# Optimization experiments

Measured on AMD Instinct MI355X. Metric: run time of the kernel, lower is better.

## Reference

```python
import jax, jax.numpy as jnp
import numpy as np

D_MODEL = 1024
N_HEADS = 16
D_HEAD = D_MODEL // N_HEADS
B, T = 4, 2048


def setup_inputs() -> dict:
    key = jax.random.key(0)
    ks = jax.random.split(key, 7)
    s = 0.02
    q = jax.random.normal(ks[0], (B, T, D_MODEL), dtype=jnp.float32)
    k = jax.random.normal(ks[1], (B, T, D_MODEL), dtype=jnp.float32)
    v = jax.random.normal(ks[2], (B, T, D_MODEL), dtype=jnp.float32)
    # causal mask, True = masked (strict upper triangle)
    mask = jnp.triu(jnp.ones((T, T), dtype=bool), k=1)[None, None, :, :]
    Wq = jax.random.normal(ks[3], (D_MODEL, D_MODEL), dtype=jnp.float32) * s
    Wk = jax.random.normal(ks[4], (D_MODEL, D_MODEL), dtype=jnp.float32) * s
    Wv = jax.random.normal(ks[5], (D_MODEL, D_MODEL), dtype=jnp.float32) * s
    Wo = jax.random.normal(ks[6], (D_MODEL, D_MODEL), dtype=jnp.float32) * s
    return {"q": q, "k": k, "v": v, "mask": mask,
            "Wq": Wq, "Wk": Wk, "Wv": Wv, "Wo": Wo}


def reference(q, k, v, mask, Wq, Wk, Wv, Wo):
    H, Dh = N_HEADS, D_HEAD
    scale = Dh ** -0.5

    def split(t):  # [B,T,D] -> [B,H,T,Dh]
        Bt, Tt, _ = t.shape
        return t.reshape(Bt, Tt, H, Dh).transpose(0, 2, 1, 3)

    # torch Linear (no bias): y = x @ W.T
    Q = split(q @ Wq.T)
    K = split(k @ Wk.T)
    V = split(v @ Wv.T)

    scores = jnp.einsum('bhqd,bhkd->bhqk', Q, K) * scale
    scores = jnp.where(mask, -jnp.inf, scores)
    attn = jax.nn.softmax(scores, axis=-1)
    attn = jnp.nan_to_num(attn)  # fully-masked rows -> 0
    out = jnp.einsum('bhqk,bhkd->bhqd', attn, V)
    out = out.transpose(0, 2, 1, 3).reshape(q.shape[0], q.shape[1], H * Dh)
    return out @ Wo.T
```

## Files before the change

### kernel.cpp

```cpp
#include <hip/hip_runtime.h>
#include <stdint.h>

#define D_MODEL 1024
#define N_HEADS 16
#define D_HEAD 64
#define BATCH 4
#define SEQ 2048
#define MTOT (BATCH * SEQ)

typedef unsigned short u16;
typedef __attribute__((ext_vector_type(8))) short bf16x8;
typedef __attribute__((ext_vector_type(4))) float f32x4;

#define MFMA(a, b, c) __builtin_amdgcn_mfma_f32_16x16x32_bf16((a), (b), (c), 0, 0, 0)

static __device__ __forceinline__ u16 f2bf(float f) {
  unsigned u = __builtin_bit_cast(unsigned, f);
  u += 0x7fffu + ((u >> 16) & 1u);
  return (u16)(u >> 16);
}

static __device__ __forceinline__ void gload_lds16(const void* g, void* l) {
  __builtin_amdgcn_global_load_lds(
      (const __attribute__((address_space(1))) void*)g,
      (__attribute__((address_space(3))) void*)l, 16, 0, 0);
}

__global__ __launch_bounds__(256) void cvt3(const float* __restrict__ a,
                                            const float* __restrict__ b,
                                            const float* __restrict__ c,
                                            u16* __restrict__ oa, u16* __restrict__ ob,
                                            u16* __restrict__ oc) {
  const int z = blockIdx.y;
  const float* in = (z == 0) ? a : (z == 1) ? b : c;
  u16* out = (z == 0) ? oa : (z == 1) ? ob : oc;
  int i = blockIdx.x * 256 + threadIdx.x;
  float4 v = ((const float4*)in)[i];
  ushort4 o;
  o.x = f2bf(v.x); o.y = f2bf(v.y); o.z = f2bf(v.z); o.w = f2bf(v.w);
  ((ushort4*)out)[i] = o;
}

__global__ __launch_bounds__(256) void cvt4(const float* __restrict__ a,
                                            const float* __restrict__ b,
                                            const float* __restrict__ c,
                                            const float* __restrict__ d,
                                            u16* __restrict__ oa, u16* __restrict__ ob,
                                            u16* __restrict__ oc, u16* __restrict__ od) {
  const int z = blockIdx.y;
  const float* in = (z == 0) ? a : (z == 1) ? b : (z == 2) ? c : d;
  u16* out = (z == 0) ? oa : (z == 1) ? ob : (z == 2) ? oc : od;
  int i = blockIdx.x * 256 + threadIdx.x;
  float4 v = ((const float4*)in)[i];
  ushort4 o;
  o.x = f2bf(v.x); o.y = f2bf(v.y); o.z = f2bf(v.z); o.w = f2bf(v.w);
  ((ushort4*)out)[i] = o;
}

__global__ __launch_bounds__(256) void gemm_qkv(const u16* __restrict__ xq,
                                                const u16* __restrict__ xk,
                                                const u16* __restrict__ xv,
                                                const u16* __restrict__ Wqb,
                                                const u16* __restrict__ Wkb,
                                                const u16* __restrict__ Wvb,
                                                u16* __restrict__ Qb, u16* __restrict__ Kb,
                                                u16* __restrict__ Vtg, int zbase) {
  __shared__ u16 As[128 * 64];
  __shared__ u16 Bs[128 * 64];
  const int z = blockIdx.z + zbase;
  const u16* A = (z == 0) ? xq : (z == 1) ? xk : xv;
  const u16* B = (z == 0) ? Wqb : (z == 1) ? Wkb : Wvb;

  const int t = threadIdx.x;
  const int lane = t & 63, wave = t >> 6;
  const int wm = wave & 1, wn = wave >> 1;
  const int lrow = lane & 15, quad = lane >> 4;
  const int m0 = blockIdx.x * 128, n0 = blockIdx.y * 128;
  const int srow = t >> 3, scol = (t & 7) * 8;

  f32x4 acc[4][4];
#pragma unroll
  for (int i = 0; i < 4; i++)
#pragma unroll
    for (int j = 0; j < 4; j++) acc[i][j] = (f32x4){0.f, 0.f, 0.f, 0.f};

  for (int k0 = 0; k0 < 1024; k0 += 64) {
#pragma unroll
    for (int r = 0; r < 4; ++r) {
      int rr = r * 32 + srow;
      gload_lds16(A + (size_t)(m0 + rr) * 1024 + k0 + scol, As + rr * 64 + scol);
      gload_lds16(B + (size_t)(n0 + rr) * 1024 + k0 + scol, Bs + rr * 64 + scol);
    }
    __syncthreads();
#pragma unroll
    for (int ks = 0; ks < 2; ++ks) {
      const int kk = ks * 32 + quad * 8;
      bf16x8 a[4], b[4];
#pragma unroll
      for (int i = 0; i < 4; i++)
        a[i] = *(const bf16x8*)(As + (wm * 64 + i * 16 + lrow) * 64 + kk);
#pragma unroll
      for (int j = 0; j < 4; j++)
        b[j] = *(const bf16x8*)(Bs + (wn * 64 + j * 16 + lrow) * 64 + kk);
#pragma unroll
      for (int i = 0; i < 4; i++)
#pragma unroll
        for (int j = 0; j < 4; j++) acc[i][j] = MFMA(a[i], b[j], acc[i][j]);
    }
    __syncthreads();
  }
  if (z == 2) {
    const int b = m0 >> 11;
    const int t0 = (m0 & 2047);
#pragma unroll
    for (int i = 0; i < 4; i++) {
      const int trow = t0 + wm * 64 + i * 16 + quad * 4;
#pragma unroll
      for (int j = 0; j < 4; j++) {
        const int n = n0 + wn * 64 + j * 16 + lrow;
        ushort4 pk;
        pk.x = f2bf(acc[i][j][0]); pk.y = f2bf(acc[i][j][1]);
        pk.z = f2bf(acc[i][j][2]); pk.w = f2bf(acc[i][j][3]);
        *(ushort4*)(Vtg + (size_t)b * D_MODEL * SEQ + (size_t)n * SEQ + trow) = pk;
      }
    }
  } else {
    u16* C = z ? Kb : Qb;
#pragma unroll
    for (int i = 0; i < 4; i++) {
      const int mr = m0 + wm * 64 + i * 16 + quad * 4;
#pragma unroll
      for (int j = 0; j < 4; j++) {
        const int n = n0 + wn * 64 + j * 16 + lrow;
#pragma unroll
        for (int r = 0; r < 4; r++) C[(size_t)(mr + r) * 1024 + n] = f2bf(acc[i][j][r]);
      }
    }
  }
}

__global__ __launch_bounds__(256) void gemm_o(const u16* __restrict__ A,
                                              const u16* __restrict__ B,
                                              float* __restrict__ C) {
  __shared__ u16 As[128 * 64];
  __shared__ u16 Bs[128 * 64];
  const int t = threadIdx.x;
  const int lane = t & 63, wave = t >> 6;
  const int wm = wave & 1, wn = wave >> 1;
  const int lrow = lane & 15, quad = lane >> 4;
  const int m0 = blockIdx.x * 128, n0 = blockIdx.y * 128;
  const int srow = t >> 3, scol = (t & 7) * 8;

  f32x4 acc[4][4];
#pragma unroll
  for (int i = 0; i < 4; i++)
#pragma unroll
    for (int j = 0; j < 4; j++) acc[i][j] = (f32x4){0.f, 0.f, 0.f, 0.f};

  for (int k0 = 0; k0 < 1024; k0 += 64) {
#pragma unroll
    for (int r = 0; r < 4; ++r) {
      int rr = r * 32 + srow;
      gload_lds16(A + (size_t)(m0 + rr) * 1024 + k0 + scol, As + rr * 64 + scol);
      gload_lds16(B + (size_t)(n0 + rr) * 1024 + k0 + scol, Bs + rr * 64 + scol);
    }
    __syncthreads();
#pragma unroll
    for (int ks = 0; ks < 2; ++ks) {
      const int kk = ks * 32 + quad * 8;
      bf16x8 a[4], b[4];
#pragma unroll
      for (int i = 0; i < 4; i++)
        a[i] = *(const bf16x8*)(As + (wm * 64 + i * 16 + lrow) * 64 + kk);
#pragma unroll
      for (int j = 0; j < 4; j++)
        b[j] = *(const bf16x8*)(Bs + (wn * 64 + j * 16 + lrow) * 64 + kk);
#pragma unroll
      for (int i = 0; i < 4; i++)
#pragma unroll
        for (int j = 0; j < 4; j++) acc[i][j] = MFMA(a[i], b[j], acc[i][j]);
    }
    __syncthreads();
  }
#pragma unroll
  for (int i = 0; i < 4; i++) {
    const int mr = m0 + wm * 64 + i * 16 + quad * 4;
#pragma unroll
    for (int j = 0; j < 4; j++) {
      const int n = n0 + wn * 64 + j * 16 + lrow;
#pragma unroll
      for (int r = 0; r < 4; r++) C[(size_t)(mr + r) * 1024 + n] = acc[i][j][r];
    }
  }
}

#define LOG2E 1.4426950408889634f
#define SC (0.125f * LOG2E)

__global__ __launch_bounds__(256) void attn_causal(const u16* __restrict__ Qb,
                                                   const u16* __restrict__ Kb,
                                                   const u16* __restrict__ Vtg,
                                                   u16* __restrict__ Ob) {
  __shared__ u16 Qs[128 * 64];
  __shared__ u16 Ks[64 * 64];
  __shared__ u16 Vs[64 * 64];
  __shared__ u16 Ps[128 * 72];

  const int t = threadIdx.x;
  const int lane = t & 63, wave = t >> 6;
  const int lrow = lane & 15, quad = lane >> 4;
  const int wb = wave * 32;
  const int bh = blockIdx.y;
  const int b = bh >> 4, h = bh & 15;
  const int col0 = h * 64;
  const size_t rowbase = (size_t)b * SEQ;
  const size_t vbase = (size_t)b * D_MODEL * SEQ;
  const int srow = t >> 3;
  const int scol = (t & 7) * 8;

  bf16x8 aOnes;
  {
    const short ov = (lrow == 0) ? (short)0x3F80 : (short)0;
#pragma unroll
    for (int e = 0; e < 8; ++e) aOnes[e] = ov;
  }

  for (int part = 0; part < 2; ++part) {
    const int qt = part ? (15 - (int)blockIdx.x) : (int)blockIdx.x;
    const int qrow0 = qt * 128;

#pragma unroll
    for (int r = 0; r < 4; ++r) {
      int rr = r * 32 + srow;
      gload_lds16(Qb + (rowbase + qrow0 + rr) * D_MODEL + col0 + scol, Qs + rr * 64 + scol);
    }

    f32x4 oacc[4][2];
    f32x4 lacc[2];
#pragma unroll
    for (int d = 0; d < 4; d++)
#pragma unroll
      for (int m = 0; m < 2; m++) oacc[d][m] = (f32x4){0.f, 0.f, 0.f, 0.f};
    lacc[0] = (f32x4){0.f, 0.f, 0.f, 0.f};
    lacc[1] = (f32x4){0.f, 0.f, 0.f, 0.f};

    const int nkt = 2 * qt + 2;
    for (int kt = 0; kt < nkt; ++kt) {
      const int j0 = kt * 64;
      __syncthreads();
#pragma unroll
      for (int r = 0; r < 2; ++r) {
        int rr = r * 32 + srow;
        gload_lds16(Kb + (rowbase + j0 + rr) * D_MODEL + col0 + scol, Ks + rr * 64 + scol);
        gload_lds16(Vtg + vbase + (size_t)(col0 + rr) * SEQ + j0 + scol, Vs + rr * 64 + scol);
      }
      __syncthreads();

      f32x4 sacc[2][4];
#pragma unroll
      for (int i = 0; i < 2; i++)
#pragma unroll
        for (int j = 0; j < 4; j++) sacc[i][j] = (f32x4){0.f, 0.f, 0.f, 0.f};
#pragma unroll
      for (int ks = 0; ks < 2; ++ks) {
        const int kk = ks * 32 + quad * 8;
        bf16x8 aq0 = *(const bf16x8*)(Qs + (wb + lrow) * 64 + kk);
        bf16x8 aq1 = *(const bf16x8*)(Qs + (wb + 16 + lrow) * 64 + kk);
#pragma unroll
        for (int jc = 0; jc < 4; jc++) {
          bf16x8 bk = *(const bf16x8*)(Ks + (jc * 16 + lrow) * 64 + kk);
          sacc[0][jc] = MFMA(aq0, bk, sacc[0][jc]);
          sacc[1][jc] = MFMA(aq1, bk, sacc[1][jc]);
        }
      }

      const bool diag = (kt >= 2 * qt);
#pragma unroll
      for (int i = 0; i < 2; i++) {
#pragma unroll
        for (int r = 0; r < 4; r++) {
          const int rloc = wb + i * 16 + quad * 4 + r;
          const int grow = qrow0 + rloc;
#pragma unroll
          for (int jc = 0; jc < 4; jc++) {
            float p = __builtin_amdgcn_exp2f(sacc[i][jc][r] * SC);
            if (diag && (j0 + jc * 16 + lrow > grow)) p = 0.f;
            Ps[rloc * 72 + jc * 16 + lrow] = f2bf(p);
          }
        }
      }

#pragma unroll
      for (int ks = 0; ks < 2; ++ks) {
        const int kk = ks * 32 + quad * 8;
        bf16x8 bP0 = *(const bf16x8*)(Ps + (wb + lrow) * 72 + kk);
        bf16x8 bP1 = *(const bf16x8*)(Ps + (wb + 16 + lrow) * 72 + kk);
        lacc[0] = MFMA(aOnes, bP0, lacc[0]);
        lacc[1] = MFMA(aOnes, bP1, lacc[1]);
#pragma unroll
        for (int d = 0; d < 4; d++) {
          bf16x8 aV = *(const bf16x8*)(Vs + (d * 16 + lrow) * 64 + kk);
          oacc[d][0] = MFMA(aV, bP0, oacc[d][0]);
          oacc[d][1] = MFMA(aV, bP1, oacc[d][1]);
        }
      }
    }
    __syncthreads();

    const float linv0 = 1.0f / __shfl(lacc[0][0], lrow);
    const float linv1 = 1.0f / __shfl(lacc[1][0], lrow);

#pragma unroll
    for (int mf = 0; mf < 2; mf++) {
      const float li = mf ? linv1 : linv0;
      u16* orow = Ob + (rowbase + qrow0 + wb + mf * 16 + lrow) * D_MODEL + col0;
#pragma unroll
      for (int d = 0; d < 4; d++) {
        f32x4 o = oacc[d][mf];
        ushort4 pk;
        pk.x = f2bf(o[0] * li); pk.y = f2bf(o[1] * li);
        pk.z = f2bf(o[2] * li); pk.w = f2bf(o[3] * li);
        *(ushort4*)(orow + d * 16 + quad * 4) = pk;
      }
    }
  }
}

extern "C" void kernel_launch(void* const* d_in, const int* in_sizes, int n_in,
                              void* d_out, int out_size, void* d_ws, size_t ws_size,
                              hipStream_t stream) {
  const float* q  = (const float*)d_in[0];
  const float* k  = (const float*)d_in[1];
  const float* v  = (const float*)d_in[2];
  const float* Wq = (const float*)d_in[4];
  const float* Wk = (const float*)d_in[5];
  const float* Wv = (const float*)d_in[6];
  const float* Wo = (const float*)d_in[7];
  float* out = (float*)d_out;

  char* ws = (char*)d_ws;
  const size_t MB = 1 << 20;
  u16* xq  = (u16*)(ws);
  u16* xk  = (u16*)(ws + 16 * MB);
  u16* xv  = (u16*)(ws + 32 * MB);
  u16* Wqb = (u16*)(ws + 48 * MB);
  u16* Wkb = (u16*)(ws + 50 * MB);
  u16* Wvb = (u16*)(ws + 52 * MB);
  u16* Wob = (u16*)(ws + 54 * MB);
  u16* Qb  = (u16*)(ws + 56 * MB);

  const dim3 cb(256);
  cvt3<<<dim3(MTOT * D_MODEL / 4 / 256, 3), cb, 0, stream>>>(q, k, v, xq, xk, xv);
  cvt4<<<dim3(D_MODEL * D_MODEL / 4 / 256, 4), cb, 0, stream>>>(Wq, Wk, Wv, Wo,
                                                                Wqb, Wkb, Wvb, Wob);

  if (ws_size >= 104 * MB) {
    u16* Kb  = (u16*)(ws + 72 * MB);
    u16* Vtg = (u16*)(ws + 88 * MB);
    gemm_qkv<<<dim3(64, 8, 3), cb, 0, stream>>>(xq, xk, xv, Wqb, Wkb, Wvb,
                                                Qb, Kb, Vtg, 0);
    attn_causal<<<dim3(8, 64), cb, 0, stream>>>(Qb, Kb, Vtg, xq);
    gemm_o<<<dim3(64, 8), cb, 0, stream>>>(xq, Wob, out);
  } else {
    u16* Kb  = (u16*)(ws);
    u16* Vtg = (u16*)(ws + 16 * MB);
    u16* Oatt = (u16*)(ws + 32 * MB);
    gemm_qkv<<<dim3(64, 8, 1), cb, 0, stream>>>(xq, xq, xq, Wqb, Wqb, Wqb,
                                                Qb, Qb, Qb, 0);
    gemm_qkv<<<dim3(64, 8, 1), cb, 0, stream>>>(xk, xk, xk, Wkb, Wkb, Wkb,
                                                Kb, Kb, Kb, 1);
    gemm_qkv<<<dim3(64, 8, 1), cb, 0, stream>>>(xv, xv, xv, Wvb, Wvb, Wvb,
                                                Vtg, Vtg, Vtg, 2);
    attn_causal<<<dim3(8, 64), cb, 0, stream>>>(Qb, Kb, Vtg, Oatt);
    gemm_o<<<dim3(64, 8), cb, 0, stream>>>(Oatt, Wob, out);
  }
}
```

Before: 361.7 us.

## Swizzle LDS layouts in GEMMs and attention, shrink attention query tile to 64

Applies an XOR swizzle to the shared-memory tiles in both GEMMs and in the attention kernel, permuting the global source column per row so MFMA operand reads avoid LDS bank conflicts. The attention kernel moves from 128-row to 64-row query tiles, one 16-row slice per wave, with twice as many blocks and finer causal balancing. P values are now truncated to bf16 instead of rounded. This adds parallelism and reduces LDS use, but each K/V tile is reused by fewer query rows, and truncation slightly changes numerics.

```diff
diff --git a/kernel.cpp b/kernel.cpp
--- a/kernel.cpp
+++ b/kernel.cpp
@@ -18,6 +18,9 @@
   unsigned u = __builtin_bit_cast(unsigned, f);
   u += 0x7fffu + ((u >> 16) & 1u);
   return (u16)(u >> 16);
+}
+static __device__ __forceinline__ u16 f2bf_t(float f) {
+  return (u16)(__builtin_bit_cast(unsigned, f) >> 16);
 }
 
 static __device__ __forceinline__ void gload_lds16(const void* g, void* l) {
@@ -57,6 +60,7 @@
   ((ushort4*)out)[i] = o;
 }
 
+
 __global__ __launch_bounds__(256) void gemm_qkv(const u16* __restrict__ xq,
                                                 const u16* __restrict__ xk,
                                                 const u16* __restrict__ xv,
@@ -76,7 +80,9 @@
   const int wm = wave & 1, wn = wave >> 1;
   const int lrow = lane & 15, quad = lane >> 4;
   const int m0 = blockIdx.x * 128, n0 = blockIdx.y * 128;
-  const int srow = t >> 3, scol = (t & 7) * 8;
+  const int srow = t >> 3;
+  const int swcol = (((t & 7) ^ (srow & 7)) << 3);
+  const int rsw = lrow & 7;
 
   f32x4 acc[4][4];
 #pragma unroll
@@ -88,20 +94,20 @@
 #pragma unroll
     for (int r = 0; r < 4; ++r) {
       int rr = r * 32 + srow;
-      gload_lds16(A + (size_t)(m0 + rr) * 1024 + k0 + scol, As + rr * 64 + scol);
-      gload_lds16(B + (size_t)(n0 + rr) * 1024 + k0 + scol, Bs + rr * 64 + scol);
+      gload_lds16(A + (size_t)(m0 + rr) * 1024 + k0 + swcol, As + rr * 64 + (t & 7) * 8);
+      gload_lds16(B + (size_t)(n0 + rr) * 1024 + k0 + swcol, Bs + rr * 64 + (t & 7) * 8);
     }
     __syncthreads();
 #pragma unroll
     for (int ks = 0; ks < 2; ++ks) {
-      const int kk = ks * 32 + quad * 8;
+      const int cx = ((ks * 4 + quad) ^ rsw) << 3;
       bf16x8 a[4], b[4];
 #pragma unroll
       for (int i = 0; i < 4; i++)
-        a[i] = *(const bf16x8*)(As + (wm * 64 + i * 16 + lrow) * 64 + kk);
+        a[i] = *(const bf16x8*)(As + (wm * 64 + i * 16 + lrow) * 64 + cx);
 #pragma unroll
       for (int j = 0; j < 4; j++)
-        b[j] = *(const bf16x8*)(Bs + (wn * 64 + j * 16 + lrow) * 64 + kk);
+        b[j] = *(const bf16x8*)(Bs + (wn * 64 + j * 16 + lrow) * 64 + cx);
 #pragma unroll
       for (int i = 0; i < 4; i++)
 #pragma unroll
@@ -149,7 +155,9 @@
   const int wm = wave & 1, wn = wave >> 1;
   const int lrow = lane & 15, quad = lane >> 4;
   const int m0 = blockIdx.x * 128, n0 = blockIdx.y * 128;
-  const int srow = t >> 3, scol = (t & 7) * 8;
+  const int srow = t >> 3;
+  const int swcol = (((t & 7) ^ (srow & 7)) << 3);
+  const int rsw = lrow & 7;
 
   f32x4 acc[4][4];
 #pragma unroll
@@ -161,20 +169,20 @@
 #pragma unroll
     for (int r = 0; r < 4; ++r) {
       int rr = r * 32 + srow;
-      gload_lds16(A + (size_t)(m0 + rr) * 1024 + k0 + scol, As + rr * 64 + scol);
-      gload_lds16(B + (size_t)(n0 + rr) * 1024 + k0 + scol, Bs + rr * 64 + scol);
+      gload_lds16(A + (size_t)(m0 + rr) * 1024 + k0 + swcol, As + rr * 64 + (t & 7) * 8);
+      gload_lds16(B + (size_t)(n0 + rr) * 1024 + k0 + swcol, Bs + rr * 64 + (t & 7) * 8);
     }
     __syncthreads();
 #pragma unroll
     for (int ks = 0; ks < 2; ++ks) {
-      const int kk = ks * 32 + quad * 8;
+      const int cx = ((ks * 4 + quad) ^ rsw) << 3;
       bf16x8 a[4], b[4];
 #pragma unroll
       for (int i = 0; i < 4; i++)
-        a[i] = *(const bf16x8*)(As + (wm * 64 + i * 16 + lrow) * 64 + kk);
+        a[i] = *(const bf16x8*)(As + (wm * 64 + i * 16 + lrow) * 64 + cx);
 #pragma unroll
       for (int j = 0; j < 4; j++)
-        b[j] = *(const bf16x8*)(Bs + (wn * 64 + j * 16 + lrow) * 64 + kk);
+        b[j] = *(const bf16x8*)(Bs + (wn * 64 + j * 16 + lrow) * 64 + cx);
 #pragma unroll
       for (int i = 0; i < 4; i++)
 #pragma unroll
@@ -201,22 +209,23 @@
                                                    const u16* __restrict__ Kb,
                                                    const u16* __restrict__ Vtg,
                                                    u16* __restrict__ Ob) {
-  __shared__ u16 Qs[128 * 64];
+  __shared__ u16 Qs[64 * 64];
   __shared__ u16 Ks[64 * 64];
   __shared__ u16 Vs[64 * 64];
-  __shared__ u16 Ps[128 * 72];
+  __shared__ u16 Ps[64 * 64];
 
   const int t = threadIdx.x;
   const int lane = t & 63, wave = t >> 6;
   const int lrow = lane & 15, quad = lane >> 4;
-  const int wb = wave * 32;
   const int bh = blockIdx.y;
   const int b = bh >> 4, h = bh & 15;
   const int col0 = h * 64;
   const size_t rowbase = (size_t)b * SEQ;
   const size_t vbase = (size_t)b * D_MODEL * SEQ;
   const int srow = t >> 3;
-  const int scol = (t & 7) * 8;
+  const int swcol = (((t & 7) ^ (srow & 7)) << 3);
+  const int pchunk = (t & 7) * 8;
+  const int rsw = lrow & 7;
 
   bf16x8 aOnes;
   {
@@ -226,102 +235,88 @@
   }
 
   for (int part = 0; part < 2; ++part) {
-    const int qt = part ? (15 - (int)blockIdx.x) : (int)blockIdx.x;
-    const int qrow0 = qt * 128;
-
-#pragma unroll
-    for (int r = 0; r < 4; ++r) {
+    const int qt = part ? (31 - (int)blockIdx.x) : (int)blockIdx.x;
+    const int qrow0 = qt * 64;
+
+#pragma unroll
+    for (int r = 0; r < 2; ++r) {
       int rr = r * 32 + srow;
-      gload_lds16(Qb + (rowbase + qrow0 + rr) * D_MODEL + col0 + scol, Qs + rr * 64 + scol);
-    }
-
-    f32x4 oacc[4][2];
-    f32x4 lacc[2];
-#pragma unroll
-    for (int d = 0; d < 4; d++)
-#pragma unroll
-      for (int m = 0; m < 2; m++) oacc[d][m] = (f32x4){0.f, 0.f, 0.f, 0.f};
-    lacc[0] = (f32x4){0.f, 0.f, 0.f, 0.f};
-    lacc[1] = (f32x4){0.f, 0.f, 0.f, 0.f};
-
-    const int nkt = 2 * qt + 2;
+      gload_lds16(Qb + (rowbase + qrow0 + rr) * D_MODEL + col0 + swcol,
+                  Qs + rr * 64 + pchunk);
+    }
+
+    f32x4 oacc[4];
+    f32x4 lacc;
+#pragma unroll
+    for (int d = 0; d < 4; d++) oacc[d] = (f32x4){0.f, 0.f, 0.f, 0.f};
+    lacc = (f32x4){0.f, 0.f, 0.f, 0.f};
+
+    const int nkt = qt + 1;
     for (int kt = 0; kt < nkt; ++kt) {
       const int j0 = kt * 64;
       __syncthreads();
 #pragma unroll
       for (int r = 0; r < 2; ++r) {
         int rr = r * 32 + srow;
-        gload_lds16(Kb + (rowbase + j0 + rr) * D_MODEL + col0 + scol, Ks + rr * 64 + scol);
-        gload_lds16(Vtg + vbase + (size_t)(col0 + rr) * SEQ + j0 + scol, Vs + rr * 64 + scol);
+        gload_lds16(Kb + (rowbase + j0 + rr) * D_MODEL + col0 + swcol,
+                    Ks + rr * 64 + pchunk);
+        gload_lds16(Vtg + vbase + (size_t)(col0 + rr) * SEQ + j0 + swcol,
+                    Vs + rr * 64 + pchunk);
       }
       __syncthreads();
 
-      f32x4 sacc[2][4];
-#pragma unroll
-      for (int i = 0; i < 2; i++)
-#pragma unroll
-        for (int j = 0; j < 4; j++) sacc[i][j] = (f32x4){0.f, 0.f, 0.f, 0.f};
+      f32x4 sacc[4];
+#pragma unroll
+      for (int j = 0; j < 4; j++) sacc[j] = (f32x4){0.f, 0.f, 0.f, 0.f};
 #pragma unroll
       for (int ks = 0; ks < 2; ++ks) {
-        const int kk = ks * 32 + quad * 8;
-        bf16x8 aq0 = *(const bf16x8*)(Qs + (wb + lrow) * 64 + kk);
-        bf16x8 aq1 = *(const bf16x8*)(Qs + (wb + 16 + lrow) * 64 + kk);
+        const int cx = ((ks * 4 + quad) ^ rsw) << 3;
+        bf16x8 aq = *(const bf16x8*)(Qs + (wave * 16 + lrow) * 64 + cx);
 #pragma unroll
         for (int jc = 0; jc < 4; jc++) {
-          bf16x8 bk = *(const bf16x8*)(Ks + (jc * 16 + lrow) * 64 + kk);
-          sacc[0][jc] = MFMA(aq0, bk, sacc[0][jc]);
-          sacc[1][jc] = MFMA(aq1, bk, sacc[1][jc]);
+          bf16x8 bk = *(const bf16x8*)(Ks + (jc * 16 + lrow) * 64 + cx);
+          sacc[jc] = MFMA(aq, bk, sacc[jc]);
         }
       }
 
-      const bool diag = (kt >= 2 * qt);
-#pragma unroll
-      for (int i = 0; i < 2; i++) {
-#pragma unroll
-        for (int r = 0; r < 4; r++) {
-          const int rloc = wb + i * 16 + quad * 4 + r;
-          const int grow = qrow0 + rloc;
-#pragma unroll
-          for (int jc = 0; jc < 4; jc++) {
-            float p = __builtin_amdgcn_exp2f(sacc[i][jc][r] * SC);
-            if (diag && (j0 + jc * 16 + lrow > grow)) p = 0.f;
-            Ps[rloc * 72 + jc * 16 + lrow] = f2bf(p);
-          }
+      const bool diag = (kt == qt);
+#pragma unroll
+      for (int r = 0; r < 4; r++) {
+        const int mrow = wave * 16 + quad * 4 + r;
+        const int grow = qrow0 + mrow;
+#pragma unroll
+        for (int jc = 0; jc < 4; jc++) {
+          float p = __builtin_amdgcn_exp2f(sacc[jc][r] * SC);
+          if (diag && (j0 + jc * 16 + lrow > grow)) p = 0.f;
+          const int cc = ((jc * 2 + (lrow >> 3)) ^ (mrow & 7)) << 3;
+          Ps[(mrow << 6) + cc + (lrow & 7)] = f2bf_t(p);
         }
       }
 
 #pragma unroll
       for (int ks = 0; ks < 2; ++ks) {
-        const int kk = ks * 32 + quad * 8;
-        bf16x8 bP0 = *(const bf16x8*)(Ps + (wb + lrow) * 72 + kk);
-        bf16x8 bP1 = *(const bf16x8*)(Ps + (wb + 16 + lrow) * 72 + kk);
-        lacc[0] = MFMA(aOnes, bP0, lacc[0]);
-        lacc[1] = MFMA(aOnes, bP1, lacc[1]);
+        const int cx = ((ks * 4 + quad) ^ rsw) << 3;
+        bf16x8 bP = *(const bf16x8*)(Ps + ((wave * 16 + lrow) << 6) + cx);
+        lacc = MFMA(aOnes, bP, lacc);
 #pragma unroll
         for (int d = 0; d < 4; d++) {
-          bf16x8 aV = *(const bf16x8*)(Vs + (d * 16 + lrow) * 64 + kk);
-          oacc[d][0] = MFMA(aV, bP0, oacc[d][0]);
-          oacc[d][1] = MFMA(aV, bP1, oacc[d][1]);
+          bf16x8 aV = *(const bf16x8*)(Vs + (d * 16 + lrow) * 64 + cx);
+          oacc[d] = MFMA(aV, bP, oacc[d]);
         }
       }
     }
     __syncthreads();
 
-    const float linv0 = 1.0f / __shfl(lacc[0][0], lrow);
-    const float linv1 = 1.0f / __shfl(lacc[1][0], lrow);
-
-#pragma unroll
-    for (int mf = 0; mf < 2; mf++) {
-      const float li = mf ? linv1 : linv0;
-      u16* orow = Ob + (rowbase + qrow0 + wb + mf * 16 + lrow) * D_MODEL + col0;
-#pragma unroll
-      for (int d = 0; d < 4; d++) {
-        f32x4 o = oacc[d][mf];
-        ushort4 pk;
-        pk.x = f2bf(o[0] * li); pk.y = f2bf(o[1] * li);
-        pk.z = f2bf(o[2] * li); pk.w = f2bf(o[3] * li);
-        *(ushort4*)(orow + d * 16 + quad * 4) = pk;
-      }
+    const float linv = 1.0f / __shfl(lacc[0], lrow);
+
+    u16* orow = Ob + (rowbase + qrow0 + wave * 16 + lrow) * D_MODEL + col0;
+#pragma unroll
+    for (int d = 0; d < 4; d++) {
+      f32x4 o = oacc[d];
+      ushort4 pk;
+      pk.x = f2bf(o[0] * linv); pk.y = f2bf(o[1] * linv);
+      pk.z = f2bf(o[2] * linv); pk.w = f2bf(o[3] * linv);
+      *(ushort4*)(orow + d * 16 + quad * 4) = pk;
     }
   }
 }
@@ -359,7 +354,7 @@
     u16* Vtg = (u16*)(ws + 88 * MB);
     gemm_qkv<<<dim3(64, 8, 3), cb, 0, stream>>>(xq, xk, xv, Wqb, Wkb, Wvb,
                                                 Qb, Kb, Vtg, 0);
-    attn_causal<<<dim3(8, 64), cb, 0, stream>>>(Qb, Kb, Vtg, xq);
+    attn_causal<<<dim3(16, 64), cb, 0, stream>>>(Qb, Kb, Vtg, xq);
     gemm_o<<<dim3(64, 8), cb, 0, stream>>>(xq, Wob, out);
   } else {
     u16* Kb  = (u16*)(ws);
@@ -371,7 +366,7 @@
                                                 Kb, Kb, Kb, 1);
     gemm_qkv<<<dim3(64, 8, 1), cb, 0, stream>>>(xv, xv, xv, Wvb, Wvb, Wvb,
                                                 Vtg, Vtg, Vtg, 2);
-    attn_causal<<<dim3(8, 64), cb, 0, stream>>>(Qb, Kb, Vtg, Oatt);
+    attn_causal<<<dim3(16, 64), cb, 0, stream>>>(Qb, Kb, Vtg, Oatt);
     gemm_o<<<dim3(64, 8), cb, 0, stream>>>(Oatt, Wob, out);
   }
 }
```

Measured after the change: 355.2 us. Within noise of the previous version (-1.8%).
